# Kernel tuning notes

Hardware: AMD Instinct MI355X
Metric: run time of the kernel (lower is better)

## Reference

```python
import jax, jax.numpy as jnp
import numpy as np

B, N, DIM, HEADS, DIM_HEAD = 8, 4096, 512, 8, 32


def next_fast_len(n):
    # smallest 5-smooth integer >= n (matches scipy.fftpack.next_fast_len)
    while True:
        m = n
        for p in (2, 3, 5):
            while m % p == 0:
                m //= p
        if m == 1:
            return n
        n += 1


def setup_inputs() -> dict:
    key = jax.random.key(0)
    ks = jax.random.split(key, 7)
    inner = HEADS * DIM_HEAD
    return {
        "x": jax.random.normal(ks[0], (B, N, DIM), dtype=jnp.float32),
        "W_in": jax.random.normal(ks[1], (DIM, inner), dtype=jnp.float32) * (1.0 / np.sqrt(DIM)),
        "b_in": jax.random.normal(ks[2], (inner,), dtype=jnp.float32) * 0.01,
        "W_out": jax.random.normal(ks[3], (inner, DIM), dtype=jnp.float32) * (1.0 / np.sqrt(inner)),
        "b_out": jax.random.normal(ks[4], (DIM,), dtype=jnp.float32) * 0.01,
        "initial_state": jax.random.normal(ks[5], (HEADS, DIM_HEAD), dtype=jnp.float32),
        "alpha_param": jax.random.normal(ks[6], (HEADS,), dtype=jnp.float32),
    }


def _conv1d_fft(x, weights):
    # x: (b, h, n, d); weights: (h, m) -> causal correlation along n
    n = x.shape[-2]
    m = weights.shape[-1]
    fast_len = next_fast_len(n + m - 1)  # static at trace time
    f_x = jnp.fft.rfft(x, n=fast_len, axis=-2)            # (b, h, f, d) complex
    f_w = jnp.fft.rfft(weights, n=fast_len, axis=-1)      # (h, f)
    prod = f_x * jnp.conj(f_w)[None, :, :, None]
    out = jnp.fft.irfft(prod, fast_len, axis=-2)          # (b, h, fast_len, d)
    out = jnp.roll(out, -1, axis=-2)
    return out[..., fast_len - n:, :]                      # (b, h, n, d)


def reference(x, W_in, b_in, W_out, b_out, initial_state, alpha_param):
    b, n, _ = x.shape
    h, dh = initial_state.shape

    xp = x @ W_in + b_in                                   # (b, n, h*dh)
    xh = xp.reshape(b, n, h, dh).transpose(0, 2, 1, 3)      # (b, h, n, dh)

    init = jnp.broadcast_to(initial_state[None, :, None, :], (b, h, 1, dh))
    xc = jnp.concatenate([init, xh], axis=2)                # (b, h, n+1, dh)
    xdiff = xc[:, :, 1:] - xc[:, :, :-1]                    # (b, h, n, dh)

    alpha = jax.nn.sigmoid(alpha_param)[:, None]            # (h, 1)
    ar = jnp.arange(n, dtype=x.dtype)
    weights = alpha * (1.0 - alpha) ** ar[::-1]             # (h, n)

    out = _conv1d_fft(xdiff, weights)                       # (b, h, n, dh)

    init_weight = (1.0 - alpha) ** (ar + 1.0)               # (h, n)
    out = out + init_weight[None, :, :, None] * initial_state[None, :, None, :]

    out = out.transpose(0, 2, 1, 3).reshape(b, n, h * dh)   # (b, n, h*dh)
    return out @ W_out + b_out
```

## Files before the change

### kernel.cpp

```cpp
#include <hip/hip_runtime.h>
#include <hip/hip_bf16.h>

typedef __attribute__((ext_vector_type(8))) short short8;
typedef __attribute__((ext_vector_type(4))) short short4v;
typedef __attribute__((ext_vector_type(4))) float f32x4;

#define NB      8
#define NSEQ    4096
#define NDIM    512
#define NHEADS  8
#define NDH     32
#define NINNER  256
#define NCHUNK  32
#define TCH     128
#define MROWS   (NB*NSEQ)

__device__ __forceinline__ short f2bf(float x) {
  union { float f; unsigned u; } v; v.f = x;
  unsigned r = (v.u + 0x7FFFu + ((v.u >> 16) & 1u)) >> 16;
  return (short)(unsigned short)r;
}
__device__ __forceinline__ float bf2f(short s) {
  union { unsigned u; float f; } v; v.u = ((unsigned)(unsigned short)s) << 16;
  return v.f;
}
__device__ __forceinline__ float sigmoidf_(float x) {
  return 1.0f / (1.0f + expf(-x));
}

__global__ __launch_bounds__(256) void wconv_kernel(
    const float* __restrict__ in, short* __restrict__ out, int K, int N)
{
  __shared__ short T[32][33];
  const int tiles_n = N >> 5;
  const int ki = blockIdx.x / tiles_n, ni = blockIdx.x % tiles_n;
  const int tx = threadIdx.x & 31, ty0 = threadIdx.x >> 5;
  #pragma unroll
  for (int r = 0; r < 4; ++r) {
    int ty = ty0 + r * 8;
    T[ty][tx] = f2bf(in[(size_t)(ki * 32 + ty) * N + ni * 32 + tx]);
  }
  __syncthreads();
  #pragma unroll
  for (int r = 0; r < 4; ++r) {
    int ty = ty0 + r * 8;
    out[(size_t)(ni * 32 + ty) * K + ki * 32 + tx] = T[tx][ty];
  }
}

__global__ __launch_bounds__(256) void gemm1_scan_kernel(
    const float* __restrict__ x, const short* __restrict__ WinT,
    const float* __restrict__ b_in, const float* __restrict__ alpha_param,
    short* __restrict__ u, float* __restrict__ Lfin)
{
  constexpr int K = NDIM, BK = 64;
  extern __shared__ char smem[];
  short (*As)[72] = reinterpret_cast<short(*)[72]>(smem);
  short (*Bs)[72] = reinterpret_cast<short(*)[72]>(smem + 128 * 72 * 2);
  float (*X)[132] = reinterpret_cast<float(*)[132]>(smem);

  const int tid = threadIdx.x;
  const int nwg = gridDim.x;
  const int tile = (blockIdx.x % 8) * (nwg / 8) + blockIdx.x / 8;
  const int bm = tile >> 1;
  const int bn = tile & 1;
  const int wave = tid >> 6, lane = tid & 63;
  const int wm = wave >> 1, wn = wave & 1;
  const int lr = lane & 15, lg = lane >> 4;

  f32x4 acc[4][4] = {};

  for (int kt = 0; kt < K; kt += BK) {
    #pragma unroll
    for (int i = 0; i < 4; ++i) {
      int idx = tid + i * 256;
      int row = idx >> 3, k8 = idx & 7;
      const float4* src = reinterpret_cast<const float4*>(
          &x[(size_t)(bm * 128 + row) * K + kt + k8 * 8]);
      float4 v0 = src[0], v1 = src[1];
      short8 s;
      s[0] = f2bf(v0.x); s[1] = f2bf(v0.y); s[2] = f2bf(v0.z); s[3] = f2bf(v0.w);
      s[4] = f2bf(v1.x); s[5] = f2bf(v1.y); s[6] = f2bf(v1.z); s[7] = f2bf(v1.w);
      *reinterpret_cast<short8*>(&As[row][k8 * 8]) = s;
    }
    #pragma unroll
    for (int i = 0; i < 4; ++i) {
      int idx = tid + i * 256;
      int n = idx >> 3, k8 = idx & 7;
      *reinterpret_cast<short8*>(&Bs[n][k8 * 8]) =
          *reinterpret_cast<const short8*>(&WinT[(size_t)(bn * 128 + n) * K + kt + k8 * 8]);
    }
    __syncthreads();
    #pragma unroll
    for (int ks = 0; ks < 2; ++ks) {
      short8 af[4], bf[4];
      #pragma unroll
      for (int m = 0; m < 4; ++m)
        af[m] = *reinterpret_cast<const short8*>(&As[wm * 64 + m * 16 + lr][ks * 32 + lg * 8]);
      #pragma unroll
      for (int n = 0; n < 4; ++n)
        bf[n] = *reinterpret_cast<const short8*>(&Bs[wn * 64 + n * 16 + lr][ks * 32 + lg * 8]);
      #pragma unroll
      for (int m = 0; m < 4; ++m)
        #pragma unroll
        for (int n = 0; n < 4; ++n)
          acc[m][n] = __builtin_amdgcn_mfma_f32_16x16x32_bf16(af[m], bf[n], acc[m][n], 0, 0, 0);
    }
    __syncthreads();
  }

  #pragma unroll
  for (int m = 0; m < 4; ++m) {
    int r0 = wm * 64 + m * 16 + lg * 4;
    #pragma unroll
    for (int n = 0; n < 4; ++n) {
      int cl = wn * 64 + n * 16 + lr;
      float bv = b_in[bn * 128 + cl];
      #pragma unroll
      for (int j = 0; j < 4; ++j) X[r0 + j][cl] = acc[m][n][j] + bv;
    }
  }
  __syncthreads();

  if (tid < 128) {
    int col = bn * 128 + tid;
    float a = sigmoidf_(alpha_param[col >> 5]);
    float cc = 1.0f - a, a2 = a * a;
    float E = 0.0f;
    for (int t0 = 0; t0 < 128; t0 += 8) {
      float xv[8], uu[8];
      #pragma unroll
      for (int i = 0; i < 8; ++i) xv[i] = X[t0 + i][tid];
      #pragma unroll
      for (int i = 0; i < 8; ++i) {
        uu[i] = fmaf(-a2, E, a * xv[i]);
        E = fmaf(cc, E, xv[i]);
      }
      #pragma unroll
      for (int i = 0; i < 8; ++i) X[t0 + i][tid] = uu[i];
    }
    Lfin[bm * 256 + col] = E;
  }
  __syncthreads();

  #pragma unroll
  for (int i = 0; i < 16; ++i) {
    int e = tid + i * 256;
    int r = e >> 5, c4 = e & 31;
    float4 v = *reinterpret_cast<const float4*>(&X[r][c4 * 4]);
    short4v s = { f2bf(v.x), f2bf(v.y), f2bf(v.z), f2bf(v.w) };
    *reinterpret_cast<short4v*>(&u[(size_t)(bm * 128 + r) * NINNER + bn * 128 + c4 * 4]) = s;
  }
}

__global__ void carry_kernel(const float* __restrict__ Lfin,
                             const float* __restrict__ init_state,
                             const float* __restrict__ alpha_param,
                             float* __restrict__ G, float* __restrict__ ccpow)
{
  int gid = blockIdx.x * 256 + threadIdx.x;
  if (blockIdx.x < 8) {
    int col = gid & 255, b = gid >> 8;
    float a = sigmoidf_(alpha_param[col >> 5]);
    float cc = 1.0f - a, a2 = a * a;
    float cT = powf(cc, 128.0f);
    float C = 0.0f, ccp = 1.0f;
    float d0 = (cc - a) * init_state[col];
    for (int c = 0; c < NCHUNK; ++c) {
      int bm = b * NCHUNK + c;
      G[bm * 256 + col] = fmaf(-a2, C, d0 * ccp);
      C = fmaf(cT, C, Lfin[bm * 256 + col]);
      ccp *= cT;
    }
  } else {
    int idx = gid - 2048;
    int h = idx >> 7, t = idx & 127;
    float a = sigmoidf_(alpha_param[h]);
    ccpow[idx] = powf(1.0f - a, (float)t);
  }
}

__global__ __launch_bounds__(256) void gemm2_kernel(
    const short* __restrict__ u, const short* __restrict__ WoutT,
    const float* __restrict__ G, const float* __restrict__ ccpow,
    const float* __restrict__ b_out, float* __restrict__ out)
{
  constexpr int K = NINNER, BK = 64, NOUT = NDIM;
  __shared__ short As[128][72];
  __shared__ short Bs[128][72];
  __shared__ float Gs[256];
  __shared__ float Ps[1024];

  const int tid = threadIdx.x;
  const int nwg = gridDim.x;
  const int tile = (blockIdx.x % 8) * (nwg / 8) + blockIdx.x / 8;
  const int bm = tile >> 2;
  const int bn = tile & 3;
  const int wave = tid >> 6, lane = tid & 63;
  const int wm = wave >> 1, wn = wave & 1;
  const int lr = lane & 15, lg = lane >> 4;

  Gs[tid] = G[bm * 256 + tid];
  #pragma unroll
  for (int i = 0; i < 4; ++i) Ps[tid + i * 256] = ccpow[tid + i * 256];
  __syncthreads();

  f32x4 acc[4][4] = {};

  for (int kt = 0; kt < K; kt += BK) {
    #pragma unroll
    for (int i = 0; i < 4; ++i) {
      int idx = tid + i * 256;
      int row = idx >> 3, k8 = idx & 7;
      int kc = kt + k8 * 8;
      short8 uv = *reinterpret_cast<const short8*>(&u[(size_t)(bm * 128 + row) * K + kc]);
      float ccp = Ps[(kc >> 5) * 128 + row];
      short8 s;
      #pragma unroll
      for (int j = 0; j < 8; ++j)
        s[j] = f2bf(fmaf(ccp, Gs[kc + j], bf2f(uv[j])));
      *reinterpret_cast<short8*>(&As[row][k8 * 8]) = s;
    }
    #pragma unroll
    for (int i = 0; i < 4; ++i) {
      int idx = tid + i * 256;
      int n = idx >> 3, k8 = idx & 7;
      *reinterpret_cast<short8*>(&Bs[n][k8 * 8]) =
          *reinterpret_cast<const short8*>(&WoutT[(size_t)(bn * 128 + n) * K + kt + k8 * 8]);
    }
    __syncthreads();
    #pragma unroll
    for (int ks = 0; ks < 2; ++ks) {
      short8 af[4], bf[4];
      #pragma unroll
      for (int m = 0; m < 4; ++m)
        af[m] = *reinterpret_cast<const short8*>(&As[wm * 64 + m * 16 + lr][ks * 32 + lg * 8]);
      #pragma unroll
      for (int n = 0; n < 4; ++n)
        bf[n] = *reinterpret_cast<const short8*>(&Bs[wn * 64 + n * 16 + lr][ks * 32 + lg * 8]);
      #pragma unroll
      for (int m = 0; m < 4; ++m)
        #pragma unroll
        for (int n = 0; n < 4; ++n)
          acc[m][n] = __builtin_amdgcn_mfma_f32_16x16x32_bf16(af[m], bf[n], acc[m][n], 0, 0, 0);
    }
    __syncthreads();
  }

  #pragma unroll
  for (int m = 0; m < 4; ++m) {
    int row0 = bm * 128 + wm * 64 + m * 16 + lg * 4;
    #pragma unroll
    for (int n = 0; n < 4; ++n) {
      int col = bn * 128 + wn * 64 + n * 16 + lr;
      float bv = b_out[col];
      #pragma unroll
      for (int j = 0; j < 4; ++j)
        out[(size_t)(row0 + j) * NOUT + col] = acc[m][n][j] + bv;
    }
  }
}

extern "C" void kernel_launch(void* const* d_in, const int* in_sizes, int n_in,
                              void* d_out, int out_size, void* d_ws, size_t ws_size,
                              hipStream_t stream)
{
  const float* x           = (const float*)d_in[0];
  const float* W_in        = (const float*)d_in[1];
  const float* b_in        = (const float*)d_in[2];
  const float* W_out       = (const float*)d_in[3];
  const float* b_out       = (const float*)d_in[4];
  const float* init_state  = (const float*)d_in[5];
  const float* alpha_param = (const float*)d_in[6];
  float* out = (float*)d_out;

  char* ws = (char*)d_ws;
  short* u      = (short*)ws;
  float* Lfin   = (float*)(ws + 16777216);
  float* G      = (float*)(ws + 16777216 + 262144);
  float* ccpow  = (float*)(ws + 16777216 + 2*262144);
  short* WinT   = (short*)(ws + 16777216 + 2*262144 + 8192);
  short* WoutT  = (short*)(ws + 16777216 + 2*262144 + 8192 + 262144);

  wconv_kernel<<<(NDIM/32)*(NINNER/32), 256, 0, stream>>>(W_in, WinT, NDIM, NINNER);
  wconv_kernel<<<(NINNER/32)*(NDIM/32), 256, 0, stream>>>(W_out, WoutT, NINNER, NDIM);

  gemm1_scan_kernel<<<(MROWS/128)*(NINNER/128), 256, 67584, stream>>>(
      x, WinT, b_in, alpha_param, u, Lfin);

  carry_kernel<<<12, 256, 0, stream>>>(Lfin, init_state, alpha_param, G, ccpow);

  gemm2_kernel<<<(MROWS/128)*(NDIM/128), 256, 0, stream>>>(
      u, WoutT, G, ccpow, b_out, out);
}
```

Baseline: 159.6 us.

## Fuse carry computation into gemm2, merge weight conversions, shrink gemm1 staging to bf16

```diff
diff --git a/kernel.cpp b/kernel.cpp
--- a/kernel.cpp
+++ b/kernel.cpp
@@ -28,40 +28,44 @@
   return 1.0f / (1.0f + expf(-x));
 }
 
-__global__ __launch_bounds__(256) void wconv_kernel(
-    const float* __restrict__ in, short* __restrict__ out, int K, int N)
+__global__ __launch_bounds__(256) void prep_kernel(
+    const float* __restrict__ W_in, const float* __restrict__ W_out,
+    short* __restrict__ WinT, short* __restrict__ WoutT)
 {
   __shared__ short T[32][33];
+  const float* src; short* dst; int K, N, tile;
+  if (blockIdx.x < 128) { src = W_in;  dst = WinT;  K = NDIM;   N = NINNER; tile = blockIdx.x; }
+  else                  { src = W_out; dst = WoutT; K = NINNER; N = NDIM;   tile = blockIdx.x - 128; }
   const int tiles_n = N >> 5;
-  const int ki = blockIdx.x / tiles_n, ni = blockIdx.x % tiles_n;
+  const int ki = tile / tiles_n, ni = tile % tiles_n;
   const int tx = threadIdx.x & 31, ty0 = threadIdx.x >> 5;
   #pragma unroll
   for (int r = 0; r < 4; ++r) {
     int ty = ty0 + r * 8;
-    T[ty][tx] = f2bf(in[(size_t)(ki * 32 + ty) * N + ni * 32 + tx]);
+    T[ty][tx] = f2bf(src[(size_t)(ki * 32 + ty) * N + ni * 32 + tx]);
   }
   __syncthreads();
   #pragma unroll
   for (int r = 0; r < 4; ++r) {
     int ty = ty0 + r * 8;
-    out[(size_t)(ni * 32 + ty) * K + ki * 32 + tx] = T[tx][ty];
-  }
-}
-
-__global__ __launch_bounds__(256) void gemm1_scan_kernel(
+    dst[(size_t)(ni * 32 + ty) * K + ki * 32 + tx] = T[tx][ty];
+  }
+}
+
+__global__ __launch_bounds__(256, 4) void gemm1_scan_kernel(
     const float* __restrict__ x, const short* __restrict__ WinT,
     const float* __restrict__ b_in, const float* __restrict__ alpha_param,
     short* __restrict__ u, float* __restrict__ Lfin)
 {
   constexpr int K = NDIM, BK = 64;
-  extern __shared__ char smem[];
-  short (*As)[72] = reinterpret_cast<short(*)[72]>(smem);
-  short (*Bs)[72] = reinterpret_cast<short(*)[72]>(smem + 128 * 72 * 2);
-  float (*X)[132] = reinterpret_cast<float(*)[132]>(smem);
+  __shared__ __align__(16) char smem[36864];
+  short (*As)[72]  = reinterpret_cast<short(*)[72]>(smem);
+  short (*Bs)[72]  = reinterpret_cast<short(*)[72]>(smem + 18432);
+  short (*X)[140]  = reinterpret_cast<short(*)[140]>(smem);
 
   const int tid = threadIdx.x;
   const int nwg = gridDim.x;
-  const int tile = (blockIdx.x % 8) * (nwg / 8) + blockIdx.x / 8;
+  const int tile = (blockIdx.x & 7) * (nwg >> 3) + (blockIdx.x >> 3);
   const int bm = tile >> 1;
   const int bn = tile & 1;
   const int wave = tid >> 6, lane = tid & 63;
@@ -117,7 +121,7 @@
       int cl = wn * 64 + n * 16 + lr;
       float bv = b_in[bn * 128 + cl];
       #pragma unroll
-      for (int j = 0; j < 4; ++j) X[r0 + j][cl] = acc[m][n][j] + bv;
+      for (int j = 0; j < 4; ++j) X[r0 + j][cl] = f2bf(acc[m][n][j] + bv);
     }
   }
   __syncthreads();
@@ -128,12 +132,13 @@
     float cc = 1.0f - a, a2 = a * a;
     float E = 0.0f;
     for (int t0 = 0; t0 < 128; t0 += 8) {
-      float xv[8], uu[8];
-      #pragma unroll
-      for (int i = 0; i < 8; ++i) xv[i] = X[t0 + i][tid];
+      float xv[8];
+      #pragma unroll
+      for (int i = 0; i < 8; ++i) xv[i] = bf2f(X[t0 + i][tid]);
+      short uu[8];
       #pragma unroll
       for (int i = 0; i < 8; ++i) {
-        uu[i] = fmaf(-a2, E, a * xv[i]);
+        uu[i] = f2bf(fmaf(-a2, E, a * xv[i]));
         E = fmaf(cc, E, xv[i]);
       }
       #pragma unroll
@@ -147,62 +152,52 @@
   for (int i = 0; i < 16; ++i) {
     int e = tid + i * 256;
     int r = e >> 5, c4 = e & 31;
-    float4 v = *reinterpret_cast<const float4*>(&X[r][c4 * 4]);
-    short4v s = { f2bf(v.x), f2bf(v.y), f2bf(v.z), f2bf(v.w) };
+    short4v s = *reinterpret_cast<const short4v*>(&X[r][c4 * 4]);
     *reinterpret_cast<short4v*>(&u[(size_t)(bm * 128 + r) * NINNER + bn * 128 + c4 * 4]) = s;
   }
 }
 
-__global__ void carry_kernel(const float* __restrict__ Lfin,
-                             const float* __restrict__ init_state,
-                             const float* __restrict__ alpha_param,
-                             float* __restrict__ G, float* __restrict__ ccpow)
-{
-  int gid = blockIdx.x * 256 + threadIdx.x;
-  if (blockIdx.x < 8) {
-    int col = gid & 255, b = gid >> 8;
-    float a = sigmoidf_(alpha_param[col >> 5]);
-    float cc = 1.0f - a, a2 = a * a;
-    float cT = powf(cc, 128.0f);
-    float C = 0.0f, ccp = 1.0f;
-    float d0 = (cc - a) * init_state[col];
-    for (int c = 0; c < NCHUNK; ++c) {
-      int bm = b * NCHUNK + c;
-      G[bm * 256 + col] = fmaf(-a2, C, d0 * ccp);
-      C = fmaf(cT, C, Lfin[bm * 256 + col]);
-      ccp *= cT;
-    }
-  } else {
-    int idx = gid - 2048;
-    int h = idx >> 7, t = idx & 127;
-    float a = sigmoidf_(alpha_param[h]);
-    ccpow[idx] = powf(1.0f - a, (float)t);
-  }
-}
-
-__global__ __launch_bounds__(256) void gemm2_kernel(
+__global__ __launch_bounds__(256, 4) void gemm2_kernel(
     const short* __restrict__ u, const short* __restrict__ WoutT,
-    const float* __restrict__ G, const float* __restrict__ ccpow,
-    const float* __restrict__ b_out, float* __restrict__ out)
+    const float* __restrict__ Lfin, const float* __restrict__ init_state,
+    const float* __restrict__ alpha_param, const float* __restrict__ b_out,
+    float* __restrict__ out)
 {
   constexpr int K = NINNER, BK = 64, NOUT = NDIM;
   __shared__ short As[128][72];
   __shared__ short Bs[128][72];
   __shared__ float Gs[256];
-  __shared__ float Ps[1024];
+  __shared__ short Ps[1024];
 
   const int tid = threadIdx.x;
   const int nwg = gridDim.x;
-  const int tile = (blockIdx.x % 8) * (nwg / 8) + blockIdx.x / 8;
+  const int tile = (blockIdx.x & 7) * (nwg >> 3) + (blockIdx.x >> 3);
   const int bm = tile >> 2;
   const int bn = tile & 3;
   const int wave = tid >> 6, lane = tid & 63;
   const int wm = wave >> 1, wn = wave & 1;
   const int lr = lane & 15, lg = lane >> 4;
 
-  Gs[tid] = G[bm * 256 + tid];
-  #pragma unroll
-  for (int i = 0; i < 4; ++i) Ps[tid + i * 256] = ccpow[tid + i * 256];
+  {
+    const int col = tid;
+    float a    = sigmoidf_(alpha_param[col >> 5]);
+    float cc   = 1.0f - a;
+    float l2cc = log2f(cc);
+    const int c = bm & 31, b = bm >> 5;
+    float cT = exp2f(128.0f * l2cc);
+    float C = 0.0f;
+    for (int j = 0; j < c; ++j)
+      C = fmaf(cT, C, Lfin[(size_t)(b * NCHUNK + j) * 256 + col]);
+    float ccpc = exp2f(128.0f * (float)c * l2cc);
+    Gs[col] = fmaf(-a * a, C, (cc - a) * init_state[col] * ccpc);
+    #pragma unroll
+    for (int i = 0; i < 4; ++i) {
+      int idx = tid + i * 256;
+      int h = idx >> 7, t = idx & 127;
+      float ah = sigmoidf_(alpha_param[h]);
+      Ps[idx] = f2bf(exp2f((float)t * log2f(1.0f - ah)));
+    }
+  }
   __syncthreads();
 
   f32x4 acc[4][4] = {};
@@ -214,7 +209,7 @@
       int row = idx >> 3, k8 = idx & 7;
       int kc = kt + k8 * 8;
       short8 uv = *reinterpret_cast<const short8*>(&u[(size_t)(bm * 128 + row) * K + kc]);
-      float ccp = Ps[(kc >> 5) * 128 + row];
+      float ccp = bf2f(Ps[(kc >> 5) * 128 + row]);
       short8 s;
       #pragma unroll
       for (int j = 0; j < 8; ++j)
@@ -275,21 +270,16 @@
   float* out = (float*)d_out;
 
   char* ws = (char*)d_ws;
-  short* u      = (short*)ws;
-  float* Lfin   = (float*)(ws + 16777216);
-  float* G      = (float*)(ws + 16777216 + 262144);
-  float* ccpow  = (float*)(ws + 16777216 + 2*262144);
-  short* WinT   = (short*)(ws + 16777216 + 2*262144 + 8192);
-  short* WoutT  = (short*)(ws + 16777216 + 2*262144 + 8192 + 262144);
-
-  wconv_kernel<<<(NDIM/32)*(NINNER/32), 256, 0, stream>>>(W_in, WinT, NDIM, NINNER);
-  wconv_kernel<<<(NINNER/32)*(NDIM/32), 256, 0, stream>>>(W_out, WoutT, NINNER, NDIM);
-
-  gemm1_scan_kernel<<<(MROWS/128)*(NINNER/128), 256, 67584, stream>>>(
+  short* u     = (short*)ws;
+  float* Lfin  = (float*)(ws + 16777216);
+  short* WinT  = (short*)(ws + 16777216 + 262144);
+  short* WoutT = (short*)(ws + 16777216 + 2 * 262144);
+
+  prep_kernel<<<256, 256, 0, stream>>>(W_in, W_out, WinT, WoutT);
+
+  gemm1_scan_kernel<<<(MROWS / 128) * (NINNER / 128), 256, 0, stream>>>(
       x, WinT, b_in, alpha_param, u, Lfin);
 
-  carry_kernel<<<12, 256, 0, stream>>>(Lfin, init_state, alpha_param, G, ccpow);
-
-  gemm2_kernel<<<(MROWS/128)*(NDIM/128), 256, 0, stream>>>(
-      u, WoutT, G, ccpow, b_out, out);
-}
+  gemm2_kernel<<<(MROWS / 128) * (NDIM / 128), 256, 0, stream>>>(
+      u, WoutT, Lfin, init_state, alpha_param, b_out, out);
+}
```

Result: slower. 165.1 us (+3.4%).
